# Performance work log

Measured on AMD Instinct MI355X. Metric: run time of the kernel, lower is better.

## Reference

```python
import jax, jax.numpy as jnp
import numpy as np

N_NODES = 100000
N_EDGES = 1600000
IN_FEATS = 128
N_HIDDEN = 128
N_CLASSES = 64


def setup_inputs() -> dict:
    key = jax.random.key(0)
    ks = jax.random.split(key, 12)
    features = jax.random.normal(ks[0], (N_NODES, IN_FEATS), dtype=jnp.float32)
    src = jax.random.randint(ks[1], (N_EDGES,), 0, N_NODES, dtype=jnp.int32)
    dst = jax.random.randint(ks[2], (N_EDGES,), 0, N_NODES, dtype=jnp.int32)
    def lin(k, fi, fo):
        s = 1.0 / np.sqrt(fi)
        kw, kb = jax.random.split(k)
        W = jax.random.uniform(kw, (fi, fo), jnp.float32, -s, s)
        b = jax.random.uniform(kb, (fo,), jnp.float32, -s, s)
        return W, b
    W1, b1 = lin(ks[3], IN_FEATS, N_HIDDEN)
    W2a, b2a = lin(ks[4], N_HIDDEN, N_HIDDEN)
    W2b, b2b = lin(ks[5], N_HIDDEN, N_HIDDEN)
    W3, b3 = lin(ks[6], N_HIDDEN, N_CLASSES)
    eps = jnp.zeros((4,), jnp.float32)  # learnable eps, one per GINConv
    return dict(features=features, src=src, dst=dst, W1=W1, b1=b1,
                W2a=W2a, b2a=b2a, W2b=W2b, b2b=b2b, W3=W3, b3=b3, eps=eps)


def _aggregate(h, src, dst, mode, deg):
    # messages flow src -> dst; h[src] is [E, d]
    msg = h[src]
    if mode == 'sum':
        return jax.ops.segment_sum(msg, dst, num_segments=N_NODES)
    if mode == 'mean':
        s = jax.ops.segment_sum(msg, dst, num_segments=N_NODES)
        return s / jnp.maximum(deg, 1.0)[:, None]
    # max: DGL yields 0 for nodes with no incoming edges
    m = jax.ops.segment_max(msg, dst, num_segments=N_NODES)
    return jnp.where(deg[:, None] > 0, m, 0.0)


def reference(features, src, dst, W1, b1, W2a, b2a, W2b, b2b, W3, b3, eps):
    deg = jax.ops.segment_sum(jnp.ones((N_EDGES,), jnp.float32), dst,
                              num_segments=N_NODES)
    h = features
    # layer 0: max aggregation + Linear + ReLU (dropout = identity in eval)
    h = (1.0 + eps[0]) * h + _aggregate(h, src, dst, 'max', deg)
    h = jax.nn.relu(h @ W1 + b1)
    # middle layers: sum aggregation + Linear + ReLU
    h = (1.0 + eps[1]) * h + _aggregate(h, src, dst, 'sum', deg)
    h = jax.nn.relu(h @ W2a + b2a)
    h = (1.0 + eps[2]) * h + _aggregate(h, src, dst, 'sum', deg)
    h = jax.nn.relu(h @ W2b + b2b)
    # output layer: mean aggregation + Linear (no activation)
    h = (1.0 + eps[3]) * h + _aggregate(h, src, dst, 'mean', deg)
    h = h @ W3 + b3
    return h
```

## Files before the change

kernel.cpp:

```cpp
#include <hip/hip_runtime.h>
#include <math.h>

#define N_NODES 100000
#define N_EDGES 1600000
#define FEAT 128
#define NBUCKET 391
#define BCAP 5120

typedef __attribute__((ext_vector_type(8))) _Float16 half8;
typedef __attribute__((ext_vector_type(4))) float floatx4;

__global__ __launch_bounds__(256) void zero_i32(int* p, int n) {
    int i = blockIdx.x * 256 + threadIdx.x;
    if (i < n) p[i] = 0;
}

__global__ __launch_bounds__(512) void bin_edges(const int* __restrict__ src,
                                                 const int* __restrict__ dst,
                                                 uint2* __restrict__ ebuf,
                                                 int* __restrict__ gcur) {
    __shared__ int hist[NBUCKET];
    __shared__ int lbase[NBUCKET];
    __shared__ int cur[NBUCKET];
    __shared__ uint2 tile[4096];

    int t = threadIdx.x;
    int e0 = blockIdx.x * 4096;
    for (int i = t; i < NBUCKET; i += 512) { hist[i] = 0; cur[i] = 0; }
    __syncthreads();

    for (int i = t; i < 4096; i += 512) {
        int e = e0 + i;
        uint2 v; v.x = 0u; v.y = 0xffffffffu;
        if (e < N_EDGES) { v.x = (unsigned)src[e]; v.y = (unsigned)dst[e]; }
        tile[i] = v;
        if (v.y != 0xffffffffu) atomicAdd(&hist[v.y >> 8], 1);
    }
    __syncthreads();

    for (int i = t; i < NBUCKET; i += 512) {
        int c = hist[i];
        lbase[i] = (c > 0) ? atomicAdd(&gcur[i], c) : 0;
    }
    __syncthreads();

    for (int i = t; i < 4096; i += 512) {
        uint2 v = tile[i];
        if (v.y == 0xffffffffu) continue;
        int b = (int)(v.y >> 8);
        int p = lbase[b] + atomicAdd(&cur[b], 1);
        if (p < BCAP) ebuf[(size_t)b * BCAP + p] = v;
    }
}

__global__ __launch_bounds__(512) void scan_buckets(const int* __restrict__ gcur,
                                                    int* __restrict__ bbase,
                                                    int* __restrict__ rowptr) {
    __shared__ int s[512];
    int t = threadIdx.x;
    int v = (t < NBUCKET) ? gcur[t] : 0;
    s[t] = v;
    __syncthreads();
    for (int off = 1; off < 512; off <<= 1) {
        int u = (t >= off) ? s[t - off] : 0;
        __syncthreads();
        s[t] += u;
        __syncthreads();
    }
    if (t < NBUCKET) bbase[t] = s[t] - v;
    if (t == 0) rowptr[N_NODES] = N_EDGES;
}

__global__ __launch_bounds__(256) void bucket_csr(const uint2* __restrict__ ebuf,
                                                  const int* __restrict__ gcur,
                                                  const int* __restrict__ bbase,
                                                  int* __restrict__ rowptr,
                                                  int* __restrict__ esrc) {
    __shared__ int cnt[256];
    __shared__ int off[256];
    __shared__ int astart[256];
    __shared__ int cur[256];

    int b = blockIdx.x, t = threadIdx.x;
    int total = gcur[b]; if (total > BCAP) total = BCAP;
    int base = bbase[b];
    const uint2* eb = ebuf + (size_t)b * BCAP;

    cnt[t] = 0; cur[t] = 0;
    __syncthreads();
    for (int i = t; i < total; i += 256) atomicAdd(&cnt[eb[i].y & 255], 1);
    __syncthreads();

    int v = cnt[t];
    off[t] = v;
    __syncthreads();
    for (int o = 1; o < 256; o <<= 1) {
        int u = (t >= o) ? off[t - o] : 0;
        __syncthreads();
        off[t] += u;
        __syncthreads();
    }
    int excl = off[t] - v;
    int node = (b << 8) + t;
    if (node < N_NODES) rowptr[node] = base + excl;
    astart[t] = base + excl;
    __syncthreads();

    for (int i = t; i < total; i += 256) {
        uint2 e = eb[i];
        int ln = (int)(e.y & 255);
        int p = astart[ln] + atomicAdd(&cur[ln], 1);
        esrc[p] = (int)e.x;
    }
}

__global__ __launch_bounds__(256) void f32_to_f16_vec(const float* __restrict__ in,
                                                      _Float16* __restrict__ out,
                                                      int n4) {
    int i = blockIdx.x * 256 + threadIdx.x;
    int stride = gridDim.x * 256;
    for (; i < n4; i += stride) {
        float4 v = ((const float4*)in)[i];
        union { uint2 u; _Float16 h[4]; } p;
        p.h[0] = (_Float16)v.x; p.h[1] = (_Float16)v.y;
        p.h[2] = (_Float16)v.z; p.h[3] = (_Float16)v.w;
        *(uint2*)(out + 4 * (size_t)i) = p.u;
    }
}

__global__ __launch_bounds__(256) void wprep(const float* __restrict__ W,
                                             _Float16* __restrict__ WT,
                                             int K, int N) {
    int idx = blockIdx.x * 256 + threadIdx.x;
    if (idx < K * N) {
        int n = idx / K, k = idx % K;
        WT[idx] = (_Float16)W[k * N + n];
    }
}

template <int MODE, int D, bool OUTF32, bool BIAS>
__global__ __launch_bounds__(256) void agg_kernel(const _Float16* __restrict__ h,
                                                  const int* __restrict__ rowptr,
                                                  const int* __restrict__ esrc,
                                                  const float* __restrict__ eps,
                                                  int ei,
                                                  const float* __restrict__ bias,
                                                  _Float16* __restrict__ outH,
                                                  float* __restrict__ outF) {
    constexpr int LPE = D / 8;
    constexpr int NG = 64 / LPE;
    int node = (int)((blockIdx.x * 256 + threadIdx.x) >> 6);
    if (node >= N_NODES) return;
    int l = threadIdx.x & 63;
    int grp = l / LPE, sl = l & (LPE - 1);
    int beg = rowptr[node], end = rowptr[node + 1];
    int deg = end - beg;

    float a[8];
#pragma unroll
    for (int i = 0; i < 8; ++i) a[i] = (MODE == 0) ? -INFINITY : 0.f;

    int e = beg;
    for (; e + 2 * NG <= end; e += 2 * NG) {
        int s0 = esrc[e + grp];
        int s1 = esrc[e + NG + grp];
        half8 v0 = *(const half8*)(h + (size_t)s0 * D + sl * 8);
        half8 v1 = *(const half8*)(h + (size_t)s1 * D + sl * 8);
#pragma unroll
        for (int i = 0; i < 8; ++i) {
            float f0 = (float)v0[i], f1 = (float)v1[i];
            if (MODE == 0) a[i] = fmaxf(a[i], fmaxf(f0, f1));
            else           a[i] += f0 + f1;
        }
    }
    for (; e < end; e += NG) {
        int ee = e + grp;
        if (ee < end) {
            int s = esrc[ee];
            half8 v = *(const half8*)(h + (size_t)s * D + sl * 8);
#pragma unroll
            for (int i = 0; i < 8; ++i) {
                float f = (float)v[i];
                if (MODE == 0) a[i] = fmaxf(a[i], f);
                else           a[i] += f;
            }
        }
    }

#pragma unroll
    for (int m = LPE; m < 64; m <<= 1) {
#pragma unroll
        for (int i = 0; i < 8; ++i) {
            float o = __shfl_xor(a[i], m, 64);
            a[i] = (MODE == 0) ? fmaxf(a[i], o) : (a[i] + o);
        }
    }

    if (grp != 0) return;
    if (MODE == 0 && deg == 0) {
#pragma unroll
        for (int i = 0; i < 8; ++i) a[i] = 0.f;
    }
    if (MODE == 2) {
        float inv = 1.f / (float)(deg > 0 ? deg : 1);
#pragma unroll
        for (int i = 0; i < 8; ++i) a[i] *= inv;
    }
    float sc = 1.f + eps[ei];
    half8 self = *(const half8*)(h + (size_t)node * D + sl * 8);
    float o[8];
#pragma unroll
    for (int i = 0; i < 8; ++i) o[i] = fmaf(sc, (float)self[i], a[i]);

    if (OUTF32) {
#pragma unroll
        for (int i = 0; i < 8; ++i)
            if (BIAS) o[i] += bias[sl * 8 + i];
        float4* dstp = (float4*)(outF + (size_t)node * D + sl * 8);
        dstp[0] = make_float4(o[0], o[1], o[2], o[3]);
        dstp[1] = make_float4(o[4], o[5], o[6], o[7]);
    } else {
        half8 ov;
#pragma unroll
        for (int i = 0; i < 8; ++i) ov[i] = (_Float16)o[i];
        *(half8*)(outH + (size_t)node * D + sl * 8) = ov;
    }
}

template <int BN, bool RELU, bool BIAS>
__global__ __launch_bounds__(256, 2) void gemm_mfma(const _Float16* __restrict__ X,
                                                    const _Float16* __restrict__ WT,
                                                    const float* __restrict__ bias,
                                                    _Float16* __restrict__ Yh) {
    __shared__ _Float16 Xs[128 * 128];
    __shared__ _Float16 Ws[BN * 128];
    char* xb = (char*)Xs;
    char* wb = (char*)Ws;

    int t = threadIdx.x;
    int l = t & 63, w = t >> 6;
    int lr = l & 15, lg = l >> 4;
    int rowBase = blockIdx.x * 128;

    {
        int row = t >> 1, hf = t & 1;
        int grow = rowBase + row;
        const char* srcp = (const char*)(X + (size_t)grow * 128 + hf * 64);
#pragma unroll
        for (int j = 0; j < 8; ++j) {
            int byte = hf * 128 + j * 16;
            half8 v = {};
            if (grow < N_NODES) v = *(const half8*)(srcp + j * 16);
            *(half8*)(xb + row * 256 + (byte ^ ((row & 7) << 4))) = v;
        }
    }
    if (t < BN * 2) {
        int row = t >> 1, hf = t & 1;
        const char* srcp = (const char*)(WT + (size_t)row * 128 + hf * 64);
#pragma unroll
        for (int j = 0; j < 8; ++j) {
            int byte = hf * 128 + j * 16;
            *(half8*)(wb + row * 256 + (byte ^ ((row & 7) << 4))) =
                *(const half8*)(srcp + j * 16);
        }
    }
    __syncthreads();

    constexpr int NCT = BN / 16;
    floatx4 acc[2][NCT];
#pragma unroll
    for (int rt = 0; rt < 2; ++rt)
#pragma unroll
        for (int ct = 0; ct < NCT; ++ct)
#pragma unroll
            for (int r = 0; r < 4; ++r) acc[rt][ct][r] = 0.f;

#pragma unroll
    for (int ks = 0; ks < 4; ++ks) {
        int kbyte = ks * 64 + lg * 16;
        half8 a[2];
#pragma unroll
        for (int rt = 0; rt < 2; ++rt) {
            int r = w * 32 + rt * 16 + lr;
            a[rt] = *(const half8*)(xb + r * 256 + (kbyte ^ ((r & 7) << 4)));
        }
#pragma unroll
        for (int ct = 0; ct < NCT; ++ct) {
            int n = ct * 16 + lr;
            half8 b = *(const half8*)(wb + n * 256 + (kbyte ^ ((n & 7) << 4)));
            acc[0][ct] = __builtin_amdgcn_mfma_f32_16x16x32_f16(a[0], b, acc[0][ct], 0, 0, 0);
            acc[1][ct] = __builtin_amdgcn_mfma_f32_16x16x32_f16(a[1], b, acc[1][ct], 0, 0, 0);
        }
    }

    float bv[NCT];
#pragma unroll
    for (int ct = 0; ct < NCT; ++ct) bv[ct] = BIAS ? bias[ct * 16 + lr] : 0.f;

    constexpr int ROWB = BN * 2;
    __syncthreads();
#pragma unroll
    for (int rt = 0; rt < 2; ++rt)
#pragma unroll
        for (int ct = 0; ct < NCT; ++ct)
#pragma unroll
            for (int r = 0; r < 4; ++r) {
                int row = w * 32 + rt * 16 + lg * 4 + r;
                int col = ct * 16 + lr;
                float v = acc[rt][ct][r] + bv[ct];
                if (RELU) v = fmaxf(v, 0.f);
                *(_Float16*)(xb + row * ROWB + ((col * 2) ^ ((row & 7) << 4))) =
                    (_Float16)v;
            }
    __syncthreads();
    {
        int row = t >> 1, hf = t & 1;
        int grow = rowBase + row;
        if (grow < N_NODES) {
            char* dstp = (char*)(Yh + (size_t)grow * BN + hf * (BN / 2));
#pragma unroll
            for (int j = 0; j < BN / 16; ++j) {
                int byte = hf * (ROWB / 2) + j * 16;
                half8 v = *(const half8*)(xb + row * ROWB + (byte ^ ((row & 7) << 4)));
                *(half8*)(dstp + j * 16) = v;
            }
        }
    }
}

extern "C" void kernel_launch(void* const* d_in, const int* in_sizes, int n_in,
                              void* d_out, int out_size, void* d_ws, size_t ws_size,
                              hipStream_t stream) {
    const float* feat = (const float*)d_in[0];
    const int*   src  = (const int*)d_in[1];
    const int*   dst  = (const int*)d_in[2];
    const float* W1   = (const float*)d_in[3];
    const float* b1   = (const float*)d_in[4];
    const float* W2a  = (const float*)d_in[5];
    const float* b2a  = (const float*)d_in[6];
    const float* W2b  = (const float*)d_in[7];
    const float* b2b  = (const float*)d_in[8];
    const float* W3   = (const float*)d_in[9];
    const float* b3   = (const float*)d_in[10];
    const float* eps  = (const float*)d_in[11];

    const size_t NH = (size_t)N_NODES * FEAT;
    char* base = (char*)d_ws;
    auto alloc = [&](size_t bytes) {
        char* p = base;
        base += (bytes + 255) & ~(size_t)255;
        return p;
    };
    _Float16* featH = (_Float16*)alloc(NH * 2);
    _Float16* hA    = (_Float16*)alloc(NH * 2);
    _Float16* hB    = (_Float16*)alloc(NH * 2);
    _Float16* WT1   = (_Float16*)alloc(128 * 128 * 2);
    _Float16* WT2a  = (_Float16*)alloc(128 * 128 * 2);
    _Float16* WT2b  = (_Float16*)alloc(128 * 128 * 2);
    _Float16* WT3   = (_Float16*)alloc(128 * 64 * 2);
    uint2* ebuf     = (uint2*)alloc((size_t)NBUCKET * BCAP * 8);
    int* rowptr     = (int*)alloc((N_NODES + 1) * 4);
    int* esrc       = (int*)alloc((size_t)N_EDGES * 4);
    int* gcur       = (int*)alloc(NBUCKET * 4);
    int* bbase      = (int*)alloc(NBUCKET * 4);

    f32_to_f16_vec<<<2048, 256, 0, stream>>>(feat, featH, (int)(NH / 4));
    wprep<<<64, 256, 0, stream>>>(W1, WT1, 128, 128);
    wprep<<<64, 256, 0, stream>>>(W2a, WT2a, 128, 128);
    wprep<<<64, 256, 0, stream>>>(W2b, WT2b, 128, 128);
    wprep<<<32, 256, 0, stream>>>(W3, WT3, 128, 64);

    zero_i32<<<(NBUCKET + 255) / 256, 256, 0, stream>>>(gcur, NBUCKET);
    bin_edges<<<(N_EDGES + 4095) / 4096, 512, 0, stream>>>(src, dst, ebuf, gcur);
    scan_buckets<<<1, 512, 0, stream>>>(gcur, bbase, rowptr);
    bucket_csr<<<NBUCKET, 256, 0, stream>>>(ebuf, gcur, bbase, rowptr, esrc);

    const int AGG_GRID = (N_NODES * 64 + 255) / 256;
    const int GEMM_GRID = (N_NODES + 127) / 128;

    agg_kernel<0, 128, false, false><<<AGG_GRID, 256, 0, stream>>>(
        featH, rowptr, esrc, eps, 0, nullptr, hB, nullptr);
    gemm_mfma<128, true, true><<<GEMM_GRID, 256, 0, stream>>>(hB, WT1, b1, hA);
    agg_kernel<1, 128, false, false><<<AGG_GRID, 256, 0, stream>>>(
        hA, rowptr, esrc, eps, 1, nullptr, hB, nullptr);
    gemm_mfma<128, true, true><<<GEMM_GRID, 256, 0, stream>>>(hB, WT2a, b2a, hA);
    agg_kernel<1, 128, false, false><<<AGG_GRID, 256, 0, stream>>>(
        hA, rowptr, esrc, eps, 2, nullptr, hB, nullptr);
    gemm_mfma<128, true, true><<<GEMM_GRID, 256, 0, stream>>>(hB, WT2b, b2b, hA);
    gemm_mfma<64, false, false><<<GEMM_GRID, 256, 0, stream>>>(hA, WT3, nullptr, hB);
    agg_kernel<2, 64, true, true><<<AGG_GRID, 256, 0, stream>>>(
        hB, rowptr, esrc, eps, 3, b3, nullptr, (float*)d_out);
}
```

Before: 387.6 us.

## Accumulate aggregation in packed fp16 and shrink GEMM row tile to 64

```diff
diff --git a/kernel.cpp b/kernel.cpp
--- a/kernel.cpp
+++ b/kernel.cpp
@@ -9,6 +9,10 @@
 
 typedef __attribute__((ext_vector_type(8))) _Float16 half8;
 typedef __attribute__((ext_vector_type(4))) float floatx4;
+
+__device__ inline half8 h8max(half8 a, half8 b) {
+    return __builtin_elementwise_max(a, b);
+}
 
 __global__ __launch_bounds__(256) void zero_i32(int* p, int n) {
     int i = blockIdx.x * 256 + threadIdx.x;
@@ -156,9 +160,8 @@
     int beg = rowptr[node], end = rowptr[node + 1];
     int deg = end - beg;
 
-    float a[8];
-#pragma unroll
-    for (int i = 0; i < 8; ++i) a[i] = (MODE == 0) ? -INFINITY : 0.f;
+    _Float16 init = (MODE == 0) ? (_Float16)(-65504.0f) : (_Float16)(0.0f);
+    half8 acc = {init, init, init, init, init, init, init, init};
 
     int e = beg;
     for (; e + 2 * NG <= end; e += 2 * NG) {
@@ -166,37 +169,35 @@
         int s1 = esrc[e + NG + grp];
         half8 v0 = *(const half8*)(h + (size_t)s0 * D + sl * 8);
         half8 v1 = *(const half8*)(h + (size_t)s1 * D + sl * 8);
-#pragma unroll
-        for (int i = 0; i < 8; ++i) {
-            float f0 = (float)v0[i], f1 = (float)v1[i];
-            if (MODE == 0) a[i] = fmaxf(a[i], fmaxf(f0, f1));
-            else           a[i] += f0 + f1;
-        }
+        if (MODE == 0) acc = h8max(acc, h8max(v0, v1));
+        else           acc += v0 + v1;
     }
     for (; e < end; e += NG) {
         int ee = e + grp;
         if (ee < end) {
             int s = esrc[ee];
             half8 v = *(const half8*)(h + (size_t)s * D + sl * 8);
-#pragma unroll
-            for (int i = 0; i < 8; ++i) {
-                float f = (float)v[i];
-                if (MODE == 0) a[i] = fmaxf(a[i], f);
-                else           a[i] += f;
-            }
-        }
-    }
-
+            if (MODE == 0) acc = h8max(acc, v);
+            else           acc += v;
+        }
+    }
+
+    union HU { half8 h; int w[4]; };
+    HU U; U.h = acc;
 #pragma unroll
     for (int m = LPE; m < 64; m <<= 1) {
-#pragma unroll
-        for (int i = 0; i < 8; ++i) {
-            float o = __shfl_xor(a[i], m, 64);
-            a[i] = (MODE == 0) ? fmaxf(a[i], o) : (a[i] + o);
-        }
+        HU V;
+#pragma unroll
+        for (int k = 0; k < 4; ++k) V.w[k] = __shfl_xor(U.w[k], m, 64);
+        if (MODE == 0) U.h = h8max(U.h, V.h);
+        else           U.h = U.h + V.h;
     }
 
     if (grp != 0) return;
+
+    float a[8];
+#pragma unroll
+    for (int i = 0; i < 8; ++i) a[i] = (float)U.h[i];
     if (MODE == 0 && deg == 0) {
 #pragma unroll
         for (int i = 0; i < 8; ++i) a[i] = 0.f;
@@ -228,11 +229,11 @@
 }
 
 template <int BN, bool RELU, bool BIAS>
-__global__ __launch_bounds__(256, 2) void gemm_mfma(const _Float16* __restrict__ X,
-                                                    const _Float16* __restrict__ WT,
-                                                    const float* __restrict__ bias,
-                                                    _Float16* __restrict__ Yh) {
-    __shared__ _Float16 Xs[128 * 128];
+__global__ __launch_bounds__(256) void gemm_mfma(const _Float16* __restrict__ X,
+                                                 const _Float16* __restrict__ WT,
+                                                 const float* __restrict__ bias,
+                                                 _Float16* __restrict__ Yh) {
+    __shared__ _Float16 Xs[64 * 128];
     __shared__ _Float16 Ws[BN * 128];
     char* xb = (char*)Xs;
     char* wb = (char*)Ws;
@@ -240,56 +241,48 @@
     int t = threadIdx.x;
     int l = t & 63, w = t >> 6;
     int lr = l & 15, lg = l >> 4;
-    int rowBase = blockIdx.x * 128;
+    int rowBase = blockIdx.x * 64;
 
     {
-        int row = t >> 1, hf = t & 1;
+        int row = t >> 2, q = t & 3;
         int grow = rowBase + row;
-        const char* srcp = (const char*)(X + (size_t)grow * 128 + hf * 64);
-#pragma unroll
-        for (int j = 0; j < 8; ++j) {
-            int byte = hf * 128 + j * 16;
+        const char* srcp = (const char*)(X + (size_t)grow * 128) + q * 64;
+#pragma unroll
+        for (int j = 0; j < 4; ++j) {
+            int byte = q * 64 + j * 16;
             half8 v = {};
             if (grow < N_NODES) v = *(const half8*)(srcp + j * 16);
             *(half8*)(xb + row * 256 + (byte ^ ((row & 7) << 4))) = v;
         }
     }
-    if (t < BN * 2) {
-        int row = t >> 1, hf = t & 1;
-        const char* srcp = (const char*)(WT + (size_t)row * 128 + hf * 64);
-#pragma unroll
-        for (int j = 0; j < 8; ++j) {
-            int byte = hf * 128 + j * 16;
+    {
+#pragma unroll
+        for (int p = 0; p < BN / 16; ++p) {
+            int idx = p * 4096 + t * 16;
+            int row = idx >> 8, byte = idx & 255;
             *(half8*)(wb + row * 256 + (byte ^ ((row & 7) << 4))) =
-                *(const half8*)(srcp + j * 16);
+                *(const half8*)((const char*)WT + idx);
         }
     }
     __syncthreads();
 
     constexpr int NCT = BN / 16;
-    floatx4 acc[2][NCT];
-#pragma unroll
-    for (int rt = 0; rt < 2; ++rt)
-#pragma unroll
-        for (int ct = 0; ct < NCT; ++ct)
-#pragma unroll
-            for (int r = 0; r < 4; ++r) acc[rt][ct][r] = 0.f;
+    floatx4 acc[NCT];
+#pragma unroll
+    for (int ct = 0; ct < NCT; ++ct)
+#pragma unroll
+        for (int r = 0; r < 4; ++r) acc[ct][r] = 0.f;
 
 #pragma unroll
     for (int ks = 0; ks < 4; ++ks) {
         int kbyte = ks * 64 + lg * 16;
-        half8 a[2];
-#pragma unroll
-        for (int rt = 0; rt < 2; ++rt) {
-            int r = w * 32 + rt * 16 + lr;
-            a[rt] = *(const half8*)(xb + r * 256 + (kbyte ^ ((r & 7) << 4)));
-        }
+        int r = w * 16 + lr;
+        half8 a = *(const half8*)(xb + r * 256 + (kbyte ^ ((r & 7) << 4)));
 #pragma unroll
         for (int ct = 0; ct < NCT; ++ct) {
             int n = ct * 16 + lr;
             half8 b = *(const half8*)(wb + n * 256 + (kbyte ^ ((n & 7) << 4)));
-            acc[0][ct] = __builtin_amdgcn_mfma_f32_16x16x32_f16(a[0], b, acc[0][ct], 0, 0, 0);
-            acc[1][ct] = __builtin_amdgcn_mfma_f32_16x16x32_f16(a[1], b, acc[1][ct], 0, 0, 0);
+            acc[ct] = __builtin_amdgcn_mfma_f32_16x16x32_f16(a, b, acc[ct], 0, 0, 0);
         }
     }
 
@@ -300,27 +293,25 @@
     constexpr int ROWB = BN * 2;
     __syncthreads();
 #pragma unroll
-    for (int rt = 0; rt < 2; ++rt)
-#pragma unroll
-        for (int ct = 0; ct < NCT; ++ct)
-#pragma unroll
-            for (int r = 0; r < 4; ++r) {
-                int row = w * 32 + rt * 16 + lg * 4 + r;
-                int col = ct * 16 + lr;
-                float v = acc[rt][ct][r] + bv[ct];
-                if (RELU) v = fmaxf(v, 0.f);
-                *(_Float16*)(xb + row * ROWB + ((col * 2) ^ ((row & 7) << 4))) =
-                    (_Float16)v;
-            }
+    for (int ct = 0; ct < NCT; ++ct)
+#pragma unroll
+        for (int r = 0; r < 4; ++r) {
+            int row = w * 16 + lg * 4 + r;
+            int col = ct * 16 + lr;
+            float v = acc[ct][r] + bv[ct];
+            if (RELU) v = fmaxf(v, 0.f);
+            *(_Float16*)(xb + row * ROWB + ((col * 2) ^ ((row & 7) << 4))) =
+                (_Float16)v;
+        }
     __syncthreads();
     {
-        int row = t >> 1, hf = t & 1;
+        int row = t >> 2, q = t & 3;
         int grow = rowBase + row;
         if (grow < N_NODES) {
-            char* dstp = (char*)(Yh + (size_t)grow * BN + hf * (BN / 2));
-#pragma unroll
-            for (int j = 0; j < BN / 16; ++j) {
-                int byte = hf * (ROWB / 2) + j * 16;
+            char* dstp = (char*)(Yh + (size_t)grow * BN) + q * (ROWB / 4);
+#pragma unroll
+            for (int j = 0; j < ROWB / 64; ++j) {
+                int byte = q * (ROWB / 4) + j * 16;
                 half8 v = *(const half8*)(xb + row * ROWB + (byte ^ ((row & 7) << 4)));
                 *(half8*)(dstp + j * 16) = v;
             }
@@ -376,7 +367,7 @@
     bucket_csr<<<NBUCKET, 256, 0, stream>>>(ebuf, gcur, bbase, rowptr, esrc);
 
     const int AGG_GRID = (N_NODES * 64 + 255) / 256;
-    const int GEMM_GRID = (N_NODES + 127) / 128;
+    const int GEMM_GRID = (N_NODES + 63) / 64;
 
     agg_kernel<0, 128, false, false><<<AGG_GRID, 256, 0, stream>>>(
         featH, rowptr, esrc, eps, 0, nullptr, hB, nullptr);
```

Measured after the change: 358.8 us. 1.08x faster.
